# Kernel optimization log

Hardware: AMD Instinct MI355X
Metric: run time of the kernel (lower is better)

## Reference

```python
import jax, jax.numpy as jnp
import numpy as np
from jax import lax

H_STARLET = jnp.array([1/16, 1/4, 3/8, 1/4, 1/16], dtype=jnp.float32)
N_SCALES = 4

def _wav_filter():
    # outer product of the 1D starlet filter -> [5,5,1,1] HWIO
    f = jnp.outer(H_STARLET, H_STARLET)
    return f[:, :, None, None]

def _analysis(image, filt, n_scales):
    """Undecimated starlet analysis: per scale, symmetric-pad, dilated conv,
    subtract. Returns list of high-freq coeffs (each same shape as image)."""
    low = image
    coeffs = []
    half = H_STARLET.shape[0] // 2  # len(filter)//2 == 2
    for i_scale in range(n_scales):
        dil = 2 ** i_scale
        p = half * dil
        padded = jnp.pad(low, ((0, 0), (p, p), (p, p), (0, 0)), mode='symmetric')
        new_low = lax.conv_general_dilated(
            padded, filt, window_strides=(1, 1), padding='VALID',
            rhs_dilation=(dil, dil),
            dimension_numbers=('NHWC', 'HWIO', 'NHWC'))
        coeffs.append(low - new_low)
        low = new_low
    return coeffs, low

def setup_inputs() -> dict:
    key = jax.random.key(0)
    k_img, k_noise = jax.random.split(key)
    image = jax.random.normal(k_img, (16, 1024, 1024, 1), dtype=jnp.float32)
    # Replicate __init__ normalization: std of each wavelet coeff of white noise.
    filt = _wav_filter()
    noise = jax.random.normal(k_noise, (1, 1024, 1024, 1), dtype=jnp.float32)
    noise_coeffs, _ = _analysis(noise, filt, N_SCALES)
    wav_norms = jnp.stack([jnp.std(c) for c in noise_coeffs])  # [n_scales]
    return {"image": image, "wav_norms": wav_norms}

def reference(image, wav_norms):
    filt = _wav_filter()
    coeffs, _ = _analysis(image, filt, N_SCALES)
    coeffs = [c / wav_norms[i] for i, c in enumerate(coeffs)]
    # coarse=False: only the n_scales high-frequency bands are returned.
    # All have identical shape (undecimated) -> stack: [n_scales, B, H, W, 1]
    return jnp.stack(coeffs)
```

## Files before the change

kernel.cpp:

```cpp
#include <hip/hip_runtime.h>


#define IMG_H 1024
#define IMG_W 1024
#define NBATCH 16
#define TILE 64

__device__ __forceinline__ int mirror_idx(int g, int n) {
    g = (g < 0) ? (-1 - g) : g;
    g = (g >= n) ? (2 * n - 1 - g) : g;
    return g;
}

template <int DIL>
__global__ __launch_bounds__(256)
void starlet_scale_kernel(const float* __restrict__ low_in,
                          const float* __restrict__ norms,
                          float* __restrict__ coeff_out,
                          float* __restrict__ low_out,
                          int scale)
{
    constexpr int R  = 2 * DIL;
    constexpr int R2 = TILE + 2 * R;
    __shared__ float lowbuf[R2 * R2];
    __shared__ float tmp[R2 * TILE];

    const int tid = threadIdx.x;
    const int tx0 = blockIdx.x * TILE;
    const int ty0 = blockIdx.y * TILE;
    const size_t img_off = (size_t)blockIdx.z * (size_t)(IMG_H * IMG_W);
    const float inv = 1.0f / norms[scale];

    for (int i = tid; i < R2 * R2; i += 256) {
        const int ry = i / R2;
        const int rx = i - ry * R2;
        const int gy = mirror_idx(ty0 - R + ry, IMG_H);
        const int gx = mirror_idx(tx0 - R + rx, IMG_W);
        lowbuf[i] = low_in[img_off + (size_t)gy * IMG_W + gx];
    }
    __syncthreads();

    for (int i = tid; i < R2 * TILE; i += 256) {
        const int y = i >> 6;
        const int x = i & (TILE - 1);
        const float* row = &lowbuf[y * R2 + x + R];
        tmp[i] = 0.375f  * row[0]
               + 0.25f   * (row[-DIL]     + row[DIL])
               + 0.0625f * (row[-2 * DIL] + row[2 * DIL]);
    }
    __syncthreads();

    for (int i = tid; i < TILE * TILE; i += 256) {
        const int y = i >> 6;
        const int x = i & (TILE - 1);
        const float* col = &tmp[(y + R) * TILE + x];
        const float nl = 0.375f  * col[0]
                       + 0.25f   * (col[-DIL * TILE]     + col[DIL * TILE])
                       + 0.0625f * (col[-2 * DIL * TILE] + col[2 * DIL * TILE]);
        const float lo = lowbuf[(y + R) * R2 + (x + R)];
        const size_t go = img_off + (size_t)(ty0 + y) * IMG_W + (tx0 + x);
        coeff_out[go] = (lo - nl) * inv;
        if (low_out) low_out[go] = nl;
    }
}

extern "C" void kernel_launch(void* const* d_in, const int* in_sizes, int n_in,
                              void* d_out, int out_size, void* d_ws, size_t ws_size,
                              hipStream_t stream) {
    const float* image = (const float*)d_in[0];
    const float* norms = (const float*)d_in[1];
    float* out = (float*)d_out;

    const size_t plane = (size_t)NBATCH * IMG_H * IMG_W;
    float* wsA = (float*)d_ws;
    float* wsB = wsA + plane;

    dim3 grid(IMG_W / TILE, IMG_H / TILE, NBATCH);
    dim3 block(256);

    starlet_scale_kernel<1><<<grid, block, 0, stream>>>(image, norms, out,             wsA,     0);
    starlet_scale_kernel<2><<<grid, block, 0, stream>>>(wsA,   norms, out + plane,     wsB,     1);
    starlet_scale_kernel<4><<<grid, block, 0, stream>>>(wsB,   norms, out + 2 * plane, wsA,     2);
    starlet_scale_kernel<8><<<grid, block, 0, stream>>>(wsA,   norms, out + 3 * plane, nullptr, 3);
}
```

Before: 452.9 us.

## Fuse all four starlet scales into one kernel with overlapping halo tiles

Replaces four per-scale launches, which write and re-read the intermediate low-pass planes through global memory, with a single kernel. Each 1024-thread block loads a 124x124 tile (64 plus a 30-pixel halo) once and computes all scales in LDS, shrinking the valid region at each step. This removes the workspace round-trips and three launches. In exchange it adds redundant halo computation, about 124 KB of LDS per block, and one block per CU.

New measurement: 503.7 us. 11.2% more time.

```diff
diff --git a/kernel.cpp b/kernel.cpp
--- a/kernel.cpp
+++ b/kernel.cpp
@@ -1,67 +1,100 @@
 #include <hip/hip_runtime.h>
 
 
-#define IMG_H 1024
-#define IMG_W 1024
-#define NBATCH 16
-#define TILE 64
+#define IMG   1024
+#define NB    16
+#define TILE  64
+#define HALO  30
+#define SPAN  124
+#define NSTAGE (SPAN * SPAN)
+#define NT    1024
 
-__device__ __forceinline__ int mirror_idx(int g, int n) {
+__device__ __forceinline__ int mirror_idx(int g) {
     g = (g < 0) ? (-1 - g) : g;
-    g = (g >= n) ? (2 * n - 1 - g) : g;
+    g = (g >= IMG) ? (2 * IMG - 1 - g) : g;
     return g;
 }
 
-template <int DIL>
-__global__ __launch_bounds__(256)
-void starlet_scale_kernel(const float* __restrict__ low_in,
+template <int D, int MIN, int MOUT>
+__device__ __forceinline__ void scale_step(float* A, float* B,
+                                           float* __restrict__ coeff, float inv,
+                                           int tid, size_t img_off, int ty0, int tx0)
+{
+    constexpr int SIN  = TILE + 2 * MIN;
+    constexpr int SOUT = TILE + 2 * MOUT;
+    constexpr int Y0   = HALO - MIN;
+    constexpr int X0   = HALO - MOUT;
+
+    for (int i = tid; i < SIN * SOUT; i += NT) {
+        const int y = Y0 + i / SOUT;
+        const int x = X0 + i % SOUT;
+        const float* a = A + y * SPAN + x;
+        B[y * SPAN + x] = 0.375f  * a[0]
+                        + 0.25f   * (a[-D]     + a[D])
+                        + 0.0625f * (a[-2 * D] + a[2 * D]);
+    }
+    __syncthreads();
+
+    for (int i = tid; i < SOUT * SOUT; i += NT) {
+        const int y = X0 + i / SOUT;
+        const int x = X0 + i % SOUT;
+        const float* b = B + y * SPAN + x;
+        const float nl = 0.375f  * b[0]
+                       + 0.25f   * (b[-D * SPAN]     + b[D * SPAN])
+                       + 0.0625f * (b[-2 * D * SPAN] + b[2 * D * SPAN]);
+        float* ap = A + y * SPAN + x;
+        const float lo = *ap;
+        *ap = nl;
+        const int oy = y - HALO, ox = x - HALO;
+        if ((unsigned)oy < TILE && (unsigned)ox < TILE) {
+            coeff[img_off + (size_t)(ty0 + oy) * IMG + (tx0 + ox)] = (lo - nl) * inv;
+        }
+    }
+    __syncthreads();
+}
+
+__global__ __launch_bounds__(NT, 1)
+void starlet_fused_kernel(const float* __restrict__ img,
                           const float* __restrict__ norms,
-                          float* __restrict__ coeff_out,
-                          float* __restrict__ low_out,
-                          int scale)
+                          float* __restrict__ out)
 {
-    constexpr int R  = 2 * DIL;
-    constexpr int R2 = TILE + 2 * R;
-    __shared__ float lowbuf[R2 * R2];
-    __shared__ float tmp[R2 * TILE];
+    __shared__ float A[NSTAGE];
+    __shared__ float B[NSTAGE];
 
     const int tid = threadIdx.x;
     const int tx0 = blockIdx.x * TILE;
     const int ty0 = blockIdx.y * TILE;
-    const size_t img_off = (size_t)blockIdx.z * (size_t)(IMG_H * IMG_W);
-    const float inv = 1.0f / norms[scale];
+    const size_t img_off = (size_t)blockIdx.z * (size_t)(IMG * IMG);
 
-    for (int i = tid; i < R2 * R2; i += 256) {
-        const int ry = i / R2;
-        const int rx = i - ry * R2;
-        const int gy = mirror_idx(ty0 - R + ry, IMG_H);
-        const int gx = mirror_idx(tx0 - R + rx, IMG_W);
-        lowbuf[i] = low_in[img_off + (size_t)gy * IMG_W + gx];
+    float r[16];
+#pragma unroll
+    for (int k = 0; k < 16; ++k) {
+        const int i = tid + k * NT;
+        if (i < NSTAGE) {
+            const int ry = i / SPAN;
+            const int rx = i - ry * SPAN;
+            const int gy = mirror_idx(ty0 - HALO + ry);
+            const int gx = mirror_idx(tx0 - HALO + rx);
+            r[k] = img[img_off + (size_t)gy * IMG + gx];
+        }
+    }
+#pragma unroll
+    for (int k = 0; k < 16; ++k) {
+        const int i = tid + k * NT;
+        if (i < NSTAGE) A[i] = r[k];
     }
     __syncthreads();
 
-    for (int i = tid; i < R2 * TILE; i += 256) {
-        const int y = i >> 6;
-        const int x = i & (TILE - 1);
-        const float* row = &lowbuf[y * R2 + x + R];
-        tmp[i] = 0.375f  * row[0]
-               + 0.25f   * (row[-DIL]     + row[DIL])
-               + 0.0625f * (row[-2 * DIL] + row[2 * DIL]);
-    }
-    __syncthreads();
+    const size_t plane = (size_t)NB * IMG * IMG;
+    const float inv0 = 1.0f / norms[0];
+    const float inv1 = 1.0f / norms[1];
+    const float inv2 = 1.0f / norms[2];
+    const float inv3 = 1.0f / norms[3];
 
-    for (int i = tid; i < TILE * TILE; i += 256) {
-        const int y = i >> 6;
-        const int x = i & (TILE - 1);
-        const float* col = &tmp[(y + R) * TILE + x];
-        const float nl = 0.375f  * col[0]
-                       + 0.25f   * (col[-DIL * TILE]     + col[DIL * TILE])
-                       + 0.0625f * (col[-2 * DIL * TILE] + col[2 * DIL * TILE]);
-        const float lo = lowbuf[(y + R) * R2 + (x + R)];
-        const size_t go = img_off + (size_t)(ty0 + y) * IMG_W + (tx0 + x);
-        coeff_out[go] = (lo - nl) * inv;
-        if (low_out) low_out[go] = nl;
-    }
+    scale_step<1, 30, 28>(A, B, out,             inv0, tid, img_off, ty0, tx0);
+    scale_step<2, 28, 24>(A, B, out + plane,     inv1, tid, img_off, ty0, tx0);
+    scale_step<4, 24, 16>(A, B, out + 2 * plane, inv2, tid, img_off, ty0, tx0);
+    scale_step<8, 16,  0>(A, B, out + 3 * plane, inv3, tid, img_off, ty0, tx0);
 }
 
 extern "C" void kernel_launch(void* const* d_in, const int* in_sizes, int n_in,
@@ -71,15 +104,7 @@
     const float* norms = (const float*)d_in[1];
     float* out = (float*)d_out;
 
-    const size_t plane = (size_t)NBATCH * IMG_H * IMG_W;
-    float* wsA = (float*)d_ws;
-    float* wsB = wsA + plane;
-
-    dim3 grid(IMG_W / TILE, IMG_H / TILE, NBATCH);
-    dim3 block(256);
-
-    starlet_scale_kernel<1><<<grid, block, 0, stream>>>(image, norms, out,             wsA,     0);
-    starlet_scale_kernel<2><<<grid, block, 0, stream>>>(wsA,   norms, out + plane,     wsB,     1);
-    starlet_scale_kernel<4><<<grid, block, 0, stream>>>(wsB,   norms, out + 2 * plane, wsA,     2);
-    starlet_scale_kernel<8><<<grid, block, 0, stream>>>(wsA,   norms, out + 3 * plane, nullptr, 3);
+    dim3 grid(IMG / TILE, IMG / TILE, NB);
+    dim3 block(NT);
+    starlet_fused_kernel<<<grid, block, 0, stream>>>(image, norms, out);
 }
```
